# Kernel tuning notes

Measured on AMD Instinct MI355X. Metric: run time of the kernel, lower is better.

## Reference

```python
import jax, jax.numpy as jnp
import numpy as np

B, T, HIN = 4, 2048, 1024
H, E = 16, 64


def setup_inputs() -> dict:
    key = jax.random.key(0)
    k1, k2, k3, k4, k5 = jax.random.split(key, 5)
    s = 1.0 / np.sqrt(HIN)
    return {
        "query": jax.random.normal(k1, (B, T, HIN), dtype=jnp.float32),
        "key_value": jax.random.normal(k2, (B, T, HIN), dtype=jnp.float32),
        "Wq": jax.random.uniform(k3, (HIN, H * E), dtype=jnp.float32, minval=-s, maxval=s),
        "Wk": jax.random.uniform(k4, (HIN, H * E), dtype=jnp.float32, minval=-s, maxval=s),
        "Wv": jax.random.uniform(k5, (HIN, H * E), dtype=jnp.float32, minval=-s, maxval=s),
    }


def reference(query, key_value, Wq, Wk, Wv):
    b, t, _ = query.shape
    scale = E ** (-0.25)  # applied to both q and k, matching e**(1/4) division
    q = (query @ Wq).reshape(b, t, H, E) * scale      # [b,t,h,e]
    k = (key_value @ Wk).reshape(b, t, H, E) * scale  # [b,t,h,e]
    v = (key_value @ Wv).reshape(b, t, H, E)          # [b,t,h,e]
    dot = jnp.einsum("bqhe,bkhe->bhqk", q, k)         # [b,h,t,t]
    attn = jax.nn.softmax(dot, axis=-1)
    out = jnp.einsum("bhqk,bkhe->bqhe", attn, v)      # [b,t,h,e]
    return out.reshape(b, t, H * E)
```

## Files before the change

### kernel.cpp

```cpp
#include <hip/hip_runtime.h>
#include <hip/hip_bf16.h>
#include <stdint.h>


typedef __bf16 bf16;
typedef __attribute__((ext_vector_type(8))) __bf16 bf16x8;
typedef __attribute__((ext_vector_type(4))) __bf16 bf16x4;
typedef __attribute__((ext_vector_type(4))) float f32x4;
typedef __attribute__((ext_vector_type(4))) short s16x4;

#define B_    4
#define T_    2048
#define HIN_  1024
#define H_    16
#define E_    64
#define NOUT_ 1024
#define LOG2E 1.4426950408889634f
#define QKSCALE 0.35355339059327373f
#define QSCALE  (QKSCALE * LOG2E)

__device__ __forceinline__ void gl_lds16(const void* g, void* l) {
  __builtin_amdgcn_global_load_lds((__attribute__((address_space(1))) void*)g,
                                   (__attribute__((address_space(3))) void*)l,
                                   16, 0, 0);
}

__global__ __launch_bounds__(256) void cvt_kernel(const float* __restrict__ Xq,
                                                  const float* __restrict__ Xkv,
                                                  bf16* __restrict__ Xb) {
  const float* src = blockIdx.y ? Xkv : Xq;
  bf16* dst = Xb + (size_t)blockIdx.y * (8192 * 1024);
  size_t i = ((size_t)blockIdx.x * 256 + threadIdx.x) * 8;
  float4 f0 = ((const float4*)(src + i))[0];
  float4 f1 = ((const float4*)(src + i))[1];
  bf16x8 t = {(bf16)f0.x, (bf16)f0.y, (bf16)f0.z, (bf16)f0.w,
              (bf16)f1.x, (bf16)f1.y, (bf16)f1.z, (bf16)f1.w};
  *(bf16x8*)(dst + i) = t;
}

__global__ __launch_bounds__(256) void wt_kernel(const float* __restrict__ Wq,
                                                 const float* __restrict__ Wk,
                                                 const float* __restrict__ Wv,
                                                 bf16* __restrict__ Wt) {
  __shared__ float s[32][33];
  const int z = blockIdx.z;
  const float* W = (z == 0) ? Wq : ((z == 1) ? Wk : Wv);
  bf16* out = Wt + (size_t)z * HIN_ * NOUT_;
  const int n0 = blockIdx.x * 32, k0 = blockIdx.y * 32;
  const int tx = threadIdx.x, ty = threadIdx.y;
#pragma unroll
  for (int i = 0; i < 4; i++)
    s[ty + i * 8][tx] = W[(size_t)(k0 + ty + i * 8) * NOUT_ + n0 + tx];
  __syncthreads();
#pragma unroll
  for (int i = 0; i < 4; i++)
    out[(size_t)(n0 + ty + i * 8) * HIN_ + k0 + tx] = (bf16)s[tx][ty + i * 8];
}

__global__ __launch_bounds__(256, 4) void proj_kernel(const bf16* __restrict__ Xb,
                                                      const bf16* __restrict__ Wt,
                                                      bf16* __restrict__ Qb,
                                                      bf16* __restrict__ Kb,
                                                      bf16* __restrict__ Vtb) {
  __shared__ bf16 As[128 * 64];
  __shared__ bf16 Bs[128 * 64];
  const int z = blockIdx.z;
  const bf16* Abase = (z == 0) ? Xb : ((z == 1) ? Xb + (size_t)8192 * 1024 : Wt + (size_t)2 * HIN_ * NOUT_);
  const bf16* Bbase = (z == 0) ? Wt : ((z == 1) ? Wt + (size_t)HIN_ * NOUT_ : Xb + (size_t)8192 * 1024);
  const int mt = (z == 2) ? blockIdx.y : blockIdx.x;
  const int nt = (z == 2) ? blockIdx.x : blockIdx.y;
  const int m0 = mt * 128, n0 = nt * 128;
  const int tid = threadIdx.x;
  const int w = tid >> 6, lane = tid & 63, quad = lane >> 4, lo = lane & 15;
  const int wm = (w >> 1) * 64, wn = (w & 1) * 64;
  const int srow = w * 8 + (lane >> 3);
  const int schunk = (lane & 7) ^ (srow & 7);

  f32x4 acc[4][4] = {};

  for (int k0 = 0; k0 < HIN_; k0 += 64) {
    __syncthreads();
#pragma unroll
    for (int j = 0; j < 4; j++) {
      int row = j * 32 + srow;
      gl_lds16(Abase + (size_t)(m0 + row) * HIN_ + k0 + schunk * 8, As + (j * 32 + w * 8) * 64);
      gl_lds16(Bbase + (size_t)(n0 + row) * HIN_ + k0 + schunk * 8, Bs + (j * 32 + w * 8) * 64);
    }
    __syncthreads();
#pragma unroll
    for (int kk = 0; kk < 2; kk++) {
      bf16x8 bfrag[4], afrag[4];
#pragma unroll
      for (int j = 0; j < 4; j++) {
        int off = ((((kk << 2) + quad) ^ (lo & 7)) << 3);
        bfrag[j] = *(const bf16x8*)(Bs + (wn + j * 16 + lo) * 64 + off);
        afrag[j] = *(const bf16x8*)(As + (wm + j * 16 + lo) * 64 + off);
      }
#pragma unroll
      for (int i = 0; i < 4; i++)
#pragma unroll
        for (int j = 0; j < 4; j++)
          acc[i][j] = __builtin_amdgcn_mfma_f32_16x16x32_bf16(afrag[i], bfrag[j], acc[i][j], 0, 0, 0);
    }
  }

#pragma unroll
  for (int i = 0; i < 4; i++)
#pragma unroll
    for (int j = 0; j < 4; j++)
#pragma unroll
      for (int r = 0; r < 4; r++) {
        int m = m0 + wm + i * 16 + quad * 4 + r;
        int n = n0 + wn + j * 16 + lo;
        float v = acc[i][j][r];
        if (z == 2) {
          int h = m >> 6, e = m & 63, b = n >> 11, t = n & 2047;
          Vtb[(((size_t)b * H_ + h) * E_ + e) * T_ + t] = (bf16)v;
        } else {
          int b = m >> 11, t = m & 2047, h = n >> 6, e = n & 63;
          if (z == 0)
            Qb[(((size_t)b * H_ + h) * T_ + t) * E_ + e] = (bf16)(v * QSCALE);
          else
            Kb[(((size_t)b * H_ + h) * T_ + t) * E_ + e] = (bf16)(v * QKSCALE);
        }
      }
}

__global__ __launch_bounds__(128, 2) void attn_kernel(const bf16* __restrict__ Qb,
                                                      const bf16* __restrict__ Kb,
                                                      const bf16* __restrict__ Vtb,
                                                      float* __restrict__ out) {
  __shared__ bf16 Ks[64 * 64];
  __shared__ bf16 Vts[64 * 64];
  const int tid = threadIdx.x;
  const int w = tid >> 6, lane = tid & 63, quad = lane >> 4, lo = lane & 15;
  const int bh = blockIdx.x, q0 = blockIdx.y * 128;
  const int wq = q0 + w * 64;
  const bf16* Qg = Qb + (size_t)bh * T_ * E_;
  const bf16* Kg = Kb + (size_t)bh * T_ * E_;
  const bf16* Vg = Vtb + (size_t)bh * E_ * T_;
  const int srow = lane >> 3;
  const int schunk = (lane & 7) ^ (srow & 7);

  bf16x8 qf[4][2];
#pragma unroll
  for (int qi = 0; qi < 4; qi++)
#pragma unroll
    for (int ks = 0; ks < 2; ks++)
      qf[qi][ks] = *(const bf16x8*)(Qg + (size_t)(wq + qi * 16 + lo) * E_ + ks * 32 + quad * 8);

  f32x4 acc[4][4] = {};
  float lsum[4] = {0.f, 0.f, 0.f, 0.f};

  for (int kt = 0; kt < T_ / 64; kt++) {
    __syncthreads();
#pragma unroll
    for (int i = 0; i < 4; i++) {
      int row = w * 32 + i * 8 + srow;
      gl_lds16(Kg + (size_t)(kt * 64 + row) * E_ + schunk * 8, Ks + (w * 32 + i * 8) * 64);
      gl_lds16(Vg + (size_t)row * T_ + kt * 64 + schunk * 8, Vts + (w * 32 + i * 8) * 64);
    }
    __syncthreads();

    bf16x8 kf[4][2];
#pragma unroll
    for (int ti = 0; ti < 4; ti++)
#pragma unroll
      for (int ks = 0; ks < 2; ks++)
        kf[ti][ks] = *(const bf16x8*)(Ks + (ti * 16 + lo) * 64 + ((((ks << 2) + quad) ^ (lo & 7)) << 3));

    bf16x4 pf[4][4];
#pragma unroll
    for (int qi = 0; qi < 4; qi++) {
      f32x4 st[4] = {};
#pragma unroll
      for (int ks = 0; ks < 2; ks++)
#pragma unroll
        for (int ti = 0; ti < 4; ti++)
          st[ti] = __builtin_amdgcn_mfma_f32_16x16x32_bf16(kf[ti][ks], qf[qi][ks], st[ti], 0, 0, 0);
      float ls = 0.f;
#pragma unroll
      for (int ti = 0; ti < 4; ti++) {
        bf16x4 p4;
#pragma unroll
        for (int r = 0; r < 4; r++) {
          float p = __builtin_amdgcn_exp2f(st[ti][r]);
          ls += p;
          p4[r] = (bf16)p;
        }
        pf[qi][ti] = p4;
      }
      lsum[qi] += ls;
    }

#pragma unroll
    for (int tc = 0; tc < 4; tc++)
#pragma unroll
      for (int ej = 0; ej < 4; ej++) {
        bf16x4 vf = *(const bf16x4*)(Vts + (ej * 16 + lo) * 64 +
                                     (((tc * 2 + (quad >> 1)) ^ (lo & 7)) << 3) + (quad & 1) * 4);
#pragma unroll
        for (int qi = 0; qi < 4; qi++)
          acc[qi][ej] = __builtin_amdgcn_mfma_f32_16x16x16bf16_1k(
              __builtin_bit_cast(s16x4, pf[qi][tc]), __builtin_bit_cast(s16x4, vf),
              acc[qi][ej], 0, 0, 0);
      }
  }

  const int b = bh >> 4, h = bh & 15;
#pragma unroll
  for (int qi = 0; qi < 4; qi++) {
    float l = lsum[qi];
    l += __shfl_xor(l, 16);
    l += __shfl_xor(l, 32);
#pragma unroll
    for (int r = 0; r < 4; r++) {
      float linv = __builtin_amdgcn_rcpf(__shfl(l, quad * 4 + r));
      size_t t = q0 + w * 64 + qi * 16 + quad * 4 + r;
#pragma unroll
      for (int ej = 0; ej < 4; ej++)
        out[((size_t)b * T_ + t) * NOUT_ + h * E_ + ej * 16 + lo] = acc[qi][ej][r] * linv;
    }
  }
}

extern "C" void kernel_launch(void* const* d_in, const int* in_sizes, int n_in,
                              void* d_out, int out_size, void* d_ws, size_t ws_size,
                              hipStream_t stream) {
  const float* Xq  = (const float*)d_in[0];
  const float* Xkv = (const float*)d_in[1];
  const float* Wq  = (const float*)d_in[2];
  const float* Wk  = (const float*)d_in[3];
  const float* Wv  = (const float*)d_in[4];
  float* out = (float*)d_out;

  char* ws = (char*)d_ws;
  bf16* Qb  = (bf16*)(ws);
  bf16* Kb  = (bf16*)(ws + ((size_t)16 << 20));
  bf16* Vtb = (bf16*)(ws + ((size_t)32 << 20));
  bf16* Wt  = (bf16*)(ws + ((size_t)48 << 20));
  bf16* Xb  = (bf16*)d_out;

  hipLaunchKernelGGL(cvt_kernel, dim3(4096, 2), dim3(256), 0, stream, Xq, Xkv, Xb);
  hipLaunchKernelGGL(wt_kernel, dim3(32, 32, 3), dim3(32, 8), 0, stream, Wq, Wk, Wv, Wt);
  hipLaunchKernelGGL(proj_kernel, dim3(64, 8, 3), dim3(256), 0, stream, Xb, Wt, Qb, Kb, Vtb);
  hipLaunchKernelGGL(attn_kernel, dim3(64, 16), dim3(128), 0, stream, Qb, Kb, Vtb, out);
}
```

Baseline: 260.7 us.

## Use single-wave attention blocks with double-buffered async V and direct K loads

The attention kernel goes from two-wave blocks to one-wave blocks. K fragments are now read straight from global memory instead of being staged through LDS. V tiles are double-buffered in LDS with asynchronous global-to-LDS loads, with the next tile prefetched while the current one is used, so all __syncthreads barriers are gone. Separately, the bf16 conversion and weight-transpose kernels are merged into one launch to save launch overhead. The risks are that K loads from global (via L2) may be exposed as latency, and that correctness depends on the compiler waiting for the async LDS writes to finish before V is read.

```diff
diff --git a/kernel.cpp b/kernel.cpp
--- a/kernel.cpp
+++ b/kernel.cpp
@@ -25,36 +25,39 @@
                                    16, 0, 0);
 }
 
-__global__ __launch_bounds__(256) void cvt_kernel(const float* __restrict__ Xq,
-                                                  const float* __restrict__ Xkv,
-                                                  bf16* __restrict__ Xb) {
-  const float* src = blockIdx.y ? Xkv : Xq;
-  bf16* dst = Xb + (size_t)blockIdx.y * (8192 * 1024);
-  size_t i = ((size_t)blockIdx.x * 256 + threadIdx.x) * 8;
-  float4 f0 = ((const float4*)(src + i))[0];
-  float4 f1 = ((const float4*)(src + i))[1];
-  bf16x8 t = {(bf16)f0.x, (bf16)f0.y, (bf16)f0.z, (bf16)f0.w,
-              (bf16)f1.x, (bf16)f1.y, (bf16)f1.z, (bf16)f1.w};
-  *(bf16x8*)(dst + i) = t;
-}
-
-__global__ __launch_bounds__(256) void wt_kernel(const float* __restrict__ Wq,
-                                                 const float* __restrict__ Wk,
-                                                 const float* __restrict__ Wv,
-                                                 bf16* __restrict__ Wt) {
+__global__ __launch_bounds__(256) void prep_kernel(const float* __restrict__ Xq,
+                                                   const float* __restrict__ Xkv,
+                                                   const float* __restrict__ Wq,
+                                                   const float* __restrict__ Wk,
+                                                   const float* __restrict__ Wv,
+                                                   bf16* __restrict__ Xb,
+                                                   bf16* __restrict__ Wt) {
   __shared__ float s[32][33];
-  const int z = blockIdx.z;
-  const float* W = (z == 0) ? Wq : ((z == 1) ? Wk : Wv);
-  bf16* out = Wt + (size_t)z * HIN_ * NOUT_;
-  const int n0 = blockIdx.x * 32, k0 = blockIdx.y * 32;
-  const int tx = threadIdx.x, ty = threadIdx.y;
-#pragma unroll
-  for (int i = 0; i < 4; i++)
-    s[ty + i * 8][tx] = W[(size_t)(k0 + ty + i * 8) * NOUT_ + n0 + tx];
-  __syncthreads();
-#pragma unroll
-  for (int i = 0; i < 4; i++)
-    out[(size_t)(n0 + ty + i * 8) * HIN_ + k0 + tx] = (bf16)s[tx][ty + i * 8];
+  const int bid = blockIdx.x, tid = threadIdx.x;
+  if (bid < 8192) {
+    const float* src = (bid < 4096) ? Xq : Xkv;
+    bf16* dst = Xb + (size_t)(bid >> 12) * (8192 * 1024);
+    size_t i = ((size_t)(bid & 4095) * 256 + tid) * 8;
+    float4 f0 = ((const float4*)(src + i))[0];
+    float4 f1 = ((const float4*)(src + i))[1];
+    bf16x8 t = {(bf16)f0.x, (bf16)f0.y, (bf16)f0.z, (bf16)f0.w,
+                (bf16)f1.x, (bf16)f1.y, (bf16)f1.z, (bf16)f1.w};
+    *(bf16x8*)(dst + i) = t;
+  } else {
+    const int wb = bid - 8192;
+    const int z = wb >> 10, r = wb & 1023;
+    const float* W = (z == 0) ? Wq : ((z == 1) ? Wk : Wv);
+    bf16* out = Wt + (size_t)z * HIN_ * NOUT_;
+    const int n0 = (r & 31) * 32, k0 = (r >> 5) * 32;
+    const int tx = tid & 31, ty = tid >> 5;
+#pragma unroll
+    for (int i = 0; i < 4; i++)
+      s[ty + i * 8][tx] = W[(size_t)(k0 + ty + i * 8) * NOUT_ + n0 + tx];
+    __syncthreads();
+#pragma unroll
+    for (int i = 0; i < 4; i++)
+      out[(size_t)(n0 + ty + i * 8) * HIN_ + k0 + tx] = (bf16)s[tx][ty + i * 8];
+  }
 }
 
 __global__ __launch_bounds__(256, 4) void proj_kernel(const bf16* __restrict__ Xb,
@@ -126,16 +129,14 @@
       }
 }
 
-__global__ __launch_bounds__(128, 2) void attn_kernel(const bf16* __restrict__ Qb,
-                                                      const bf16* __restrict__ Kb,
-                                                      const bf16* __restrict__ Vtb,
-                                                      float* __restrict__ out) {
-  __shared__ bf16 Ks[64 * 64];
-  __shared__ bf16 Vts[64 * 64];
-  const int tid = threadIdx.x;
-  const int w = tid >> 6, lane = tid & 63, quad = lane >> 4, lo = lane & 15;
-  const int bh = blockIdx.x, q0 = blockIdx.y * 128;
-  const int wq = q0 + w * 64;
+__global__ __launch_bounds__(64, 2) void attn_kernel(const bf16* __restrict__ Qb,
+                                                     const bf16* __restrict__ Kb,
+                                                     const bf16* __restrict__ Vtb,
+                                                     float* __restrict__ out) {
+  __shared__ bf16 Vts[2][64 * 64];
+  const int lane = threadIdx.x;
+  const int quad = lane >> 4, lo = lane & 15;
+  const int bh = blockIdx.x, wq = blockIdx.y * 64;
   const bf16* Qg = Qb + (size_t)bh * T_ * E_;
   const bf16* Kg = Kb + (size_t)bh * T_ * E_;
   const bf16* Vg = Vtb + (size_t)bh * E_ * T_;
@@ -149,25 +150,20 @@
     for (int ks = 0; ks < 2; ks++)
       qf[qi][ks] = *(const bf16x8*)(Qg + (size_t)(wq + qi * 16 + lo) * E_ + ks * 32 + quad * 8);
 
+#pragma unroll
+  for (int i = 0; i < 8; i++)
+    gl_lds16(Vg + (size_t)(i * 8 + srow) * T_ + schunk * 8, &Vts[0][i * 8 * 64]);
+
   f32x4 acc[4][4] = {};
   float lsum[4] = {0.f, 0.f, 0.f, 0.f};
 
-  for (int kt = 0; kt < T_ / 64; kt++) {
-    __syncthreads();
-#pragma unroll
-    for (int i = 0; i < 4; i++) {
-      int row = w * 32 + i * 8 + srow;
-      gl_lds16(Kg + (size_t)(kt * 64 + row) * E_ + schunk * 8, Ks + (w * 32 + i * 8) * 64);
-      gl_lds16(Vg + (size_t)row * T_ + kt * 64 + schunk * 8, Vts + (w * 32 + i * 8) * 64);
-    }
-    __syncthreads();
-
+  for (int kt = 0; kt < 32; kt++) {
     bf16x8 kf[4][2];
 #pragma unroll
     for (int ti = 0; ti < 4; ti++)
 #pragma unroll
       for (int ks = 0; ks < 2; ks++)
-        kf[ti][ks] = *(const bf16x8*)(Ks + (ti * 16 + lo) * 64 + ((((ks << 2) + quad) ^ (lo & 7)) << 3));
+        kf[ti][ks] = *(const bf16x8*)(Kg + (size_t)(kt * 64 + ti * 16 + lo) * E_ + ks * 32 + quad * 8);
 
     bf16x4 pf[4][4];
 #pragma unroll
@@ -193,11 +189,12 @@
       lsum[qi] += ls;
     }
 
+    const bf16* vb = &Vts[kt & 1][0];
 #pragma unroll
     for (int tc = 0; tc < 4; tc++)
 #pragma unroll
       for (int ej = 0; ej < 4; ej++) {
-        bf16x4 vf = *(const bf16x4*)(Vts + (ej * 16 + lo) * 64 +
+        bf16x4 vf = *(const bf16x4*)(vb + (ej * 16 + lo) * 64 +
                                      (((tc * 2 + (quad >> 1)) ^ (lo & 7)) << 3) + (quad & 1) * 4);
 #pragma unroll
         for (int qi = 0; qi < 4; qi++)
@@ -205,6 +202,12 @@
               __builtin_bit_cast(s16x4, pf[qi][tc]), __builtin_bit_cast(s16x4, vf),
               acc[qi][ej], 0, 0, 0);
       }
+
+    const int nt = (kt + 1) & 31;
+    bf16* dst = &Vts[(kt + 1) & 1][0];
+#pragma unroll
+    for (int i = 0; i < 8; i++)
+      gl_lds16(Vg + (size_t)(i * 8 + srow) * T_ + nt * 64 + schunk * 8, dst + i * 8 * 64);
   }
 
   const int b = bh >> 4, h = bh & 15;
@@ -216,7 +219,7 @@
 #pragma unroll
     for (int r = 0; r < 4; r++) {
       float linv = __builtin_amdgcn_rcpf(__shfl(l, quad * 4 + r));
-      size_t t = q0 + w * 64 + qi * 16 + quad * 4 + r;
+      size_t t = wq + qi * 16 + quad * 4 + r;
 #pragma unroll
       for (int ej = 0; ej < 4; ej++)
         out[((size_t)b * T_ + t) * NOUT_ + h * E_ + ej * 16 + lo] = acc[qi][ej][r] * linv;
@@ -241,8 +244,7 @@
   bf16* Wt  = (bf16*)(ws + ((size_t)48 << 20));
   bf16* Xb  = (bf16*)d_out;
 
-  hipLaunchKernelGGL(cvt_kernel, dim3(4096, 2), dim3(256), 0, stream, Xq, Xkv, Xb);
-  hipLaunchKernelGGL(wt_kernel, dim3(32, 32, 3), dim3(32, 8), 0, stream, Wq, Wk, Wv, Wt);
+  hipLaunchKernelGGL(prep_kernel, dim3(11264), dim3(256), 0, stream, Xq, Xkv, Wq, Wk, Wv, Xb, Wt);
   hipLaunchKernelGGL(proj_kernel, dim3(64, 8, 3), dim3(256), 0, stream, Xb, Wt, Qb, Kb, Vtb);
-  hipLaunchKernelGGL(attn_kernel, dim3(64, 16), dim3(128), 0, stream, Qb, Kb, Vtb, out);
-}
+  hipLaunchKernelGGL(attn_kernel, dim3(64, 32), dim3(64), 0, stream, Qb, Kb, Vtb, out);
+}
```

Result: slower. 268.8 us (+3.1%).
